# Kernel tuning notes

Measured on AMD Instinct MI355X. Metric: run time of the kernel, lower is better.

The kernel has to match this reference:

```python
import jax, jax.numpy as jnp
import numpy as np

N_COARSE = 100_000
M_FINE = 4 * N_COARSE
GRID = 128
C_IN, C_HID, C_OUT = 32, 64, 32
K3 = 27   # 3x3x3 neighborhood
K2 = 8    # 2x2x2 transposed-conv offsets


def setup_inputs() -> dict:
    rng = np.random.default_rng(0)
    # --- sparse coarse grid: N unique voxels in GRID^3 ---
    lin = np.sort(rng.choice(GRID ** 3, size=N_COARSE, replace=False))
    cx, cy, cz = lin // (GRID * GRID), (lin // GRID) % GRID, lin % GRID
    coords = np.stack([cx, cy, cz], 1).astype(np.int64)
    # --- rulebook: neighbor index per voxel per 3^3 offset (sentinel = N) ---
    offs = np.array([(dx, dy, dz) for dx in (-1, 0, 1) for dy in (-1, 0, 1) for dz in (-1, 0, 1)])
    nbr = np.full((N_COARSE, K3), N_COARSE, np.int32)
    for k in range(K3):
        nc = coords + offs[k]
        valid = ((nc >= 0) & (nc < GRID)).all(1)
        nlin = nc[:, 0] * GRID * GRID + nc[:, 1] * GRID + nc[:, 2]
        pos = np.clip(np.searchsorted(lin, nlin), 0, N_COARSE - 1)
        found = valid & (lin[pos] == nlin)
        nbr[found, k] = pos[found].astype(np.int32)
    # --- fine grid: 4 distinct children (of 8) per coarse voxel ---
    child = np.argsort(rng.random((N_COARSE, K2)), axis=1)[:, :4].astype(np.int32)
    parent_idx = np.repeat(np.arange(N_COARSE, dtype=np.int32), 4)
    offset_idx = child.reshape(-1)

    key = jax.random.key(0)
    ks = jax.random.split(key, 16)
    nrm = lambda k, sh, fan: (jax.random.normal(k, sh, jnp.float32) / np.sqrt(fan)).astype(jnp.float32)
    return {
        "feats_in": jax.random.normal(ks[0], (N_COARSE, C_IN), jnp.float32),
        "x_up_feats": jax.random.normal(ks[1], (M_FINE, C_OUT), jnp.float32),
        "nbr_idx": jnp.asarray(nbr),
        "parent_idx": jnp.asarray(parent_idx),
        "offset_idx": jnp.asarray(offset_idx),
        "W_enc1": nrm(ks[2], (K3, C_IN, C_HID), K3 * C_IN),
        "b_enc1": jnp.zeros((C_HID,), jnp.float32),
        "W_enc2": nrm(ks[3], (K3, C_HID, C_HID), K3 * C_HID),
        "b_enc2": jnp.zeros((C_HID,), jnp.float32),
        "W_enc3": nrm(ks[4], (K3, C_HID, C_HID), K3 * C_HID),
        "b_enc3": jnp.zeros((C_HID,), jnp.float32),
        "W_t": nrm(ks[5], (K2, C_HID, C_HID), C_HID),
        "b_t": jnp.zeros((C_HID,), jnp.float32),
        "W_d1": nrm(ks[6], (C_HID, C_HID), C_HID),
        "b_d1": jnp.zeros((C_HID,), jnp.float32),
        "W_d2": nrm(ks[7], (C_HID, C_OUT), C_HID),
        "b_d2": jnp.zeros((C_OUT,), jnp.float32),
    }


def _sparse_conv3(x, nbr, W, b):
    """3x3x3 stride-1 sparse conv: gather neighbors, per-offset matmul, accumulate.
    x: [N,Cin], nbr: [N,27] (sentinel N -> zero feature), W: [27,Cin,Cout]."""
    xp = jnp.concatenate([x, jnp.zeros((1, x.shape[1]), x.dtype)], 0)  # sentinel row
    acc = jnp.broadcast_to(b, (x.shape[0], W.shape[-1]))
    for k in range(W.shape[0]):  # fixed 27-way structural loop
        acc = acc + xp[nbr[:, k]] @ W[k]
    return acc


def _t_conv2(x, parent_idx, offset_idx, W, b):
    """2x2x2 stride-2 transposed sparse conv onto a given fine grid.
    x: [N,C], parent_idx: [M] (sentinel N), offset_idx: [M] in [0,8)."""
    xp = jnp.concatenate([x, jnp.zeros((1, x.shape[1]), x.dtype)], 0)
    g = xp[parent_idx]  # [M,C]
    out = jnp.broadcast_to(b, (g.shape[0], W.shape[-1]))
    for k in range(W.shape[0]):  # fixed 8-way structural loop
        out = out + jnp.where((offset_idx == k)[:, None], g @ W[k], 0.0)
    return out


def reference(feats_in, x_up_feats, nbr_idx, parent_idx, offset_idx,
              W_enc1, b_enc1, W_enc2, b_enc2, W_enc3, b_enc3,
              W_t, b_t, W_d1, b_d1, W_d2, b_d2):
    # encoder: (conv -> dropout[eval: identity] -> relu) x 3
    x = jax.nn.relu(_sparse_conv3(feats_in, nbr_idx, W_enc1, b_enc1))
    x = jax.nn.relu(_sparse_conv3(x, nbr_idx, W_enc2, b_enc2))
    x = jax.nn.relu(_sparse_conv3(x, nbr_idx, W_enc3, b_enc3))
    # transposed upsample conv onto x_upsample's grid
    x = _t_conv2(x, parent_idx, offset_idx, W_t, b_t)
    # decoder: relu -> 1x1 conv -> relu -> 1x1 conv, then residual add
    x = jax.nn.relu(x) @ W_d1 + b_d1
    x = jax.nn.relu(x) @ W_d2 + b_d2
    return x + x_up_feats
```

## Files before the change

kernel.cpp:

```cpp
#include <hip/hip_runtime.h>
#include <hip/hip_bf16.h>

#define NC 100000
#define MF 400000
#define K3 27

typedef __bf16 bf16_t;
typedef bf16_t bf16x8 __attribute__((ext_vector_type(8)));
typedef float  f32x4  __attribute__((ext_vector_type(4)));

#define O_E1 0
#define O_E2 55296
#define O_E3 165888
#define O_T  276480
#define O_D1 309248
#define O_D2 313344
#define W_TOTAL 315392

__device__ __align__(16) bf16_t g_w[W_TOTAL];
__device__ __align__(16) bf16_t g_x0[(size_t)NC * 32];
__device__ __align__(16) bf16_t g_x1[(size_t)NC * 64];
__device__ __align__(16) bf16_t g_x2[(size_t)NC * 64];
__device__ int g_nbrT[(size_t)K3 * NC];

static __device__ __forceinline__ bf16x8 zero8() {
    bf16x8 v;
#pragma unroll
    for (int i = 0; i < 8; ++i) v[i] = (bf16_t)0.0f;
    return v;
}

__global__ __launch_bounds__(256) void prep_k(
    const float* __restrict__ W_e1, const float* __restrict__ W_e2,
    const float* __restrict__ W_e3, const float* __restrict__ W_t,
    const float* __restrict__ W_d1, const float* __restrict__ W_d2,
    const float* __restrict__ feats, const int* __restrict__ nbr)
{
    int b = blockIdx.x;
    if (b < 154) {
        int tid = b * 256 + threadIdx.x;
        int lane = tid & 63;
        int f = tid >> 6;
        const float* src; int doff, nt, nc, fb;
        if      (f < 108) { src = W_e1; doff = O_E1; nt = 4; nc = 1; fb = 0;   }
        else if (f < 324) { src = W_e2; doff = O_E2; nt = 4; nc = 2; fb = 108; }
        else if (f < 540) { src = W_e3; doff = O_E3; nt = 4; nc = 2; fb = 324; }
        else if (f < 604) { src = W_t;  doff = O_T;  nt = 4; nc = 2; fb = 540; }
        else if (f < 612) { src = W_d1; doff = O_D1; nt = 4; nc = 2; fb = 604; }
        else              { src = W_d2; doff = O_D2; nt = 2; nc = 2; fb = 612; }
        int lf = f - fb;
        int t  = lf % nt;
        int c  = (lf / nt) % nc;
        int ko = lf / (nt * nc);
        int Cin = nc * 32, Cout = nt * 16;
        int n  = t * 16 + (lane & 15);
        int kb = c * 32 + (lane >> 4) * 8;
        bf16x8 tmp;
#pragma unroll
        for (int j = 0; j < 8; ++j)
            tmp[j] = (bf16_t)src[((size_t)ko * Cin + (kb + j)) * Cout + n];
        *(bf16x8*)(g_w + doff + (size_t)lf * 512 + lane * 8) = tmp;
    } else if (b < 1717) {
        int i = (b - 154) * 256 + threadIdx.x;
        if (i < NC * 32 / 8) {
            const f32x4* p = (const f32x4*)(feats + (size_t)i * 8);
            f32x4 lo = p[0], hi = p[1];
            bf16x8 v;
#pragma unroll
            for (int j = 0; j < 4; ++j) { v[j] = (bf16_t)lo[j]; v[j + 4] = (bf16_t)hi[j]; }
            *(bf16x8*)(g_x0 + (size_t)i * 8) = v;
        }
    } else {
        int r = (b - 1717) * 256 + threadIdx.x;
        if (r < NC) {
#pragma unroll
            for (int k = 0; k < K3; ++k)
                g_nbrT[(size_t)k * NC + r] = nbr[(size_t)r * K3 + k];
        }
    }
}

#define TS 72
template <int CH>
__global__ __launch_bounds__(128) void conv_k(
    int w_off,
    const float* __restrict__ bias,
    int src_sel, int dst_sel)
{
    constexpr int CIN = CH * 32;
    const bf16_t* xb = (src_sel == 0) ? g_x0 : (src_sel == 1 ? g_x1 : g_x2);
    bf16_t* y = (dst_sel == 1) ? g_x1 : g_x2;
    const bf16_t* wsrc = g_w + w_off;

    __shared__ __align__(16) bf16_t bB[2][4096];
    int tid = threadIdx.x;
    int wv = tid >> 6, lane = tid & 63;
    int cl = lane & 15, q = lane >> 4;

    int per = gridDim.x >> 3;
    int blk = (blockIdx.x & 7) * per + (blockIdx.x >> 3);
    int base = (blk * 2 + wv) * 64;

    {
        const bf16x8* s = (const bf16x8*)wsrc;
        bf16x8* d = (bf16x8*)bB[0];
#pragma unroll
        for (int i = 0; i < CH * 2; ++i) d[i * 128 + tid] = s[i * 128 + tid];
    }
    __syncthreads();

    f32x4 acc[4][4];
#pragma unroll
    for (int t = 0; t < 4; ++t) {
        float b = bias[t * 16 + cl];
#pragma unroll
        for (int mt = 0; mt < 4; ++mt) acc[mt][t] = (f32x4){b, b, b, b};
    }

    for (int ko = 0; ko < K3; ++ko) {
        int cur = ko & 1;
        if (ko + 1 < K3) {
            const bf16x8* s = (const bf16x8*)(wsrc + (size_t)(ko + 1) * CH * 2048);
            bf16x8* d = (bf16x8*)bB[cur ^ 1];
#pragma unroll
            for (int i = 0; i < CH * 2; ++i) d[i * 128 + tid] = s[i * 128 + tid];
        }
        int idx[4];
#pragma unroll
        for (int mt = 0; mt < 4; ++mt) {
            int r = base + mt * 16 + cl;
            idx[mt] = (r < NC) ? g_nbrT[(size_t)ko * NC + r] : NC;
        }
#pragma unroll
        for (int c = 0; c < CH; ++c) {
            bf16x8 bfr[4];
#pragma unroll
            for (int t = 0; t < 4; ++t)
                bfr[t] = *(const bf16x8*)&bB[cur][(c * 4 + t) * 512 + lane * 8];
#pragma unroll
            for (int mt = 0; mt < 4; ++mt) {
                bool valid = (unsigned)idx[mt] < (unsigned)NC;
                int s = valid ? idx[mt] : 0;
                bf16x8 a = *(const bf16x8*)(xb + (size_t)s * CIN + c * 32 + q * 8);
                if (!valid) a = zero8();
#pragma unroll
                for (int t = 0; t < 4; ++t)
                    acc[mt][t] = __builtin_amdgcn_mfma_f32_16x16x32_bf16(
                        a, bfr[t], acc[mt][t], 0, 0, 0);
            }
        }
        __syncthreads();
    }

    bf16_t* tb = ((bf16_t*)bB) + wv * 2304;
#pragma unroll
    for (int ch = 0; ch < 2; ++ch) {
#pragma unroll
        for (int mt2 = 0; mt2 < 2; ++mt2)
#pragma unroll
            for (int t = 0; t < 4; ++t)
#pragma unroll
                for (int r = 0; r < 4; ++r) {
                    float v = acc[ch * 2 + mt2][t][r];
                    v = v > 0.0f ? v : 0.0f;
                    tb[(mt2 * 16 + q * 4 + r) * TS + t * 16 + cl] = (bf16_t)v;
                }
#pragma unroll
        for (int i = 0; i < 4; ++i) {
            int rl = i * 8 + (lane >> 3);
            int c8 = (lane & 7) * 8;
            bf16x8 v8 = *(const bf16x8*)&tb[rl * TS + c8];
            int orow = base + ch * 32 + rl;
            if (orow < NC)
                *(bf16x8*)(y + (size_t)orow * 64 + c8) = v8;
        }
    }
}

#define HS 72
__global__ __launch_bounds__(256) void tconv_dec_k(
    const int*   __restrict__ offs,
    const float* __restrict__ b_t,
    const float* __restrict__ b_d1,
    const float* __restrict__ b_d2,
    const float* __restrict__ x_up,
    float*       __restrict__ out)
{
    __shared__ __align__(16) bf16_t h_lds[4][64 * HS];
    __shared__ __align__(16) int off_lds[4][64];
    int wv = threadIdx.x >> 6, lane = threadIdx.x & 63;
    int cl = lane & 15, q = lane >> 4;
    int per = gridDim.x >> 3;
    int blk = (blockIdx.x & 7) * per + (blockIdx.x >> 3);
    int p0 = (blk * 4 + wv) * 16;
    int fbase = p0 * 4;

    {
        int fi = fbase + lane;
        off_lds[wv][lane] = (fi < MF) ? offs[fi] : 0;
    }
    int code[4];
#pragma unroll
    for (int r = 0; r < 4; ++r) {
        int4 o = *(const int4*)&off_lds[wv][(q * 4 + r) * 4];
        code[r] = (1 << (4 * o.x)) | (2 << (4 * o.y)) |
                  (3 << (4 * o.z)) | (4 << (4 * o.w));
    }

    bool pv = (p0 + cl) < NC;
    size_t xrow = (size_t)(pv ? p0 + cl : 0) * 64;
    bf16x8 ax[2];
#pragma unroll
    for (int c = 0; c < 2; ++c) {
        bf16x8 t8 = *(const bf16x8*)(g_x1 + xrow + c * 32 + q * 8);
        ax[c] = pv ? t8 : zero8();
    }

    const bf16_t* wt = g_w + O_T;
#pragma unroll
    for (int k = 0; k < 8; ++k) {
        f32x4 acc[4];
#pragma unroll
        for (int t = 0; t < 4; ++t) {
            float b = b_t[t * 16 + cl];
            acc[t] = (f32x4){b, b, b, b};
        }
#pragma unroll
        for (int c = 0; c < 2; ++c) {
            const bf16_t* wb = wt + ((size_t)(k * 2 + c) * 4) * 512 + lane * 8;
#pragma unroll
            for (int t = 0; t < 4; ++t) {
                bf16x8 b = *(const bf16x8*)(wb + t * 512);
                acc[t] = __builtin_amdgcn_mfma_f32_16x16x32_bf16(ax[c], b, acc[t], 0, 0, 0);
            }
        }
#pragma unroll
        for (int r = 0; r < 4; ++r) {
            int nib = (code[r] >> (4 * k)) & 0xF;
            if (nib) {
                int fl = (((q * 4 + r) * 4) + (nib - 1)) & 63;
#pragma unroll
                for (int t = 0; t < 4; ++t) {
                    float v = acc[t][r];
                    v = v > 0.0f ? v : 0.0f;
                    h_lds[wv][fl * HS + t * 16 + cl] = (bf16_t)v;
                }
            }
        }
    }

    bf16x8 a1[4][2];
#pragma unroll
    for (int mt = 0; mt < 4; ++mt)
#pragma unroll
        for (int c = 0; c < 2; ++c)
            a1[mt][c] = *(const bf16x8*)&h_lds[wv][(mt * 16 + cl) * HS + c * 32 + q * 8];

#pragma unroll
    for (int mt = 0; mt < 4; ++mt) {
        f32x4 acc2[4];
#pragma unroll
        for (int t = 0; t < 4; ++t) {
            float b = b_d1[t * 16 + cl];
            acc2[t] = (f32x4){b, b, b, b};
        }
#pragma unroll
        for (int c = 0; c < 2; ++c)
#pragma unroll
            for (int t = 0; t < 4; ++t) {
                bf16x8 b = *(const bf16x8*)(g_w + O_D1 + (size_t)(c * 4 + t) * 512 + lane * 8);
                acc2[t] = __builtin_amdgcn_mfma_f32_16x16x32_bf16(a1[mt][c], b, acc2[t], 0, 0, 0);
            }
#pragma unroll
        for (int t = 0; t < 4; ++t)
#pragma unroll
            for (int r = 0; r < 4; ++r) {
                float v = acc2[t][r];
                v = v > 0.0f ? v : 0.0f;
                h_lds[wv][(mt * 16 + q * 4 + r) * HS + t * 16 + cl] = (bf16_t)v;
            }
    }

    float* fW = (float*)h_lds[wv];
#pragma unroll
    for (int mt = 0; mt < 4; ++mt) {
        bf16x8 a2[2];
#pragma unroll
        for (int c = 0; c < 2; ++c)
            a2[c] = *(const bf16x8*)&h_lds[wv][(mt * 16 + cl) * HS + c * 32 + q * 8];
        f32x4 acc3[2];
#pragma unroll
        for (int t = 0; t < 2; ++t) {
            float b = b_d2[t * 16 + cl];
            acc3[t] = (f32x4){b, b, b, b};
        }
#pragma unroll
        for (int c = 0; c < 2; ++c)
#pragma unroll
            for (int t = 0; t < 2; ++t) {
                bf16x8 b = *(const bf16x8*)(g_w + O_D2 + (size_t)(c * 2 + t) * 512 + lane * 8);
                acc3[t] = __builtin_amdgcn_mfma_f32_16x16x32_bf16(a2[c], b, acc3[t], 0, 0, 0);
            }
#pragma unroll
        for (int t = 0; t < 2; ++t)
#pragma unroll
            for (int r = 0; r < 4; ++r)
                fW[(mt * 16 + q * 4 + r) * 36 + t * 16 + cl] = acc3[t][r];
    }

#pragma unroll
    for (int i = 0; i < 8; ++i) {
        int rl = i * 8 + (lane >> 3);
        int c4 = (lane & 7) * 4;
        int fg = fbase + rl;
        if (fg < MF) {
            f32x4 xv = *(const f32x4*)(x_up + (size_t)fg * 32 + c4);
            f32x4 v = *(const f32x4*)&fW[rl * 36 + c4];
            v += xv;
            *(f32x4*)(out + (size_t)fg * 32 + c4) = v;
        }
    }
}

extern "C" void kernel_launch(void* const* d_in, const int* in_sizes, int n_in,
                              void* d_out, int out_size, void* d_ws, size_t ws_size,
                              hipStream_t stream) {
    const float* feats  = (const float*)d_in[0];
    const float* x_up   = (const float*)d_in[1];
    const int*   nbr    = (const int*)d_in[2];
    const int*   offs   = (const int*)d_in[4];
    const float* W_e1 = (const float*)d_in[5];
    const float* b_e1 = (const float*)d_in[6];
    const float* W_e2 = (const float*)d_in[7];
    const float* b_e2 = (const float*)d_in[8];
    const float* W_e3 = (const float*)d_in[9];
    const float* b_e3 = (const float*)d_in[10];
    const float* W_t  = (const float*)d_in[11];
    const float* b_t  = (const float*)d_in[12];
    const float* W_d1 = (const float*)d_in[13];
    const float* b_d1 = (const float*)d_in[14];
    const float* W_d2 = (const float*)d_in[15];
    const float* b_d2 = (const float*)d_in[16];
    float* out = (float*)d_out;

    prep_k<<<2108, 256, 0, stream>>>(W_e1, W_e2, W_e3, W_t, W_d1, W_d2, feats, nbr);

    conv_k<1><<<784, 128, 0, stream>>>(O_E1, b_e1, 0, 1);
    conv_k<2><<<784, 128, 0, stream>>>(O_E2, b_e2, 1, 2);
    conv_k<2><<<784, 128, 0, stream>>>(O_E3, b_e3, 2, 1);

    tconv_dec_k<<<1568, 256, 0, stream>>>(offs, b_t, b_d1, b_d2, x_up, out);
}
```

Measured before the change: 339.3 us.

## Software-pipeline neighbor gathers in sparse conv and prefetch residual input

The conv kernel now double-buffers the neighbor indices and the gathered activation fragments in registers, loading offset k+1's A tiles and offset k+2's indices while the MFMAs for offset k run. This is meant to hide the latency of the irregular global gathers. The launch bound adds a minimum-blocks hint of 1, and the extra register buffers may lower occupancy. The tconv/decoder kernel also loads the x_up residual at kernel start so that read overlaps with the compute.

Result: no change. 337.8 us (-0.4%).

```diff
diff --git a/kernel.cpp b/kernel.cpp
--- a/kernel.cpp
+++ b/kernel.cpp
@@ -81,8 +81,55 @@
 }
 
 #define TS 72
+
+#define CSTEP(KO, P) do {                                                      \
+    if ((KO) + 1 < K3) {                                                       \
+                            \
+        const bf16x8* s_ = (const bf16x8*)(wsrc + (size_t)((KO) + 1) * CH * 2048); \
+        bf16x8* d_ = (bf16x8*)bB[(P) ^ 1];                                     \
+        _Pragma("unroll")                                                      \
+        for (int i_ = 0; i_ < CH * 2; ++i_)                                    \
+            d_[i_ * 128 + tid] = s_[i_ * 128 + tid];                           \
+                 \
+        _Pragma("unroll")                                                      \
+        for (int c_ = 0; c_ < CH; ++c_)                                        \
+            _Pragma("unroll")                                                  \
+            for (int mt_ = 0; mt_ < 4; ++mt_) {                                \
+                int ii_ = idxbuf[(P) ^ 1][mt_];                                \
+                bool va_ = (unsigned)ii_ < (unsigned)NC;                       \
+                int ss_ = va_ ? ii_ : 0;                                       \
+                bf16x8 a_ = *(const bf16x8*)(xb + (size_t)ss_ * CIN + c_ * 32 + q * 8); \
+                if (!va_) a_ = zero8();                                        \
+                abuf[(P) ^ 1][c_][mt_] = a_;                                   \
+            }                                                                  \
+    }                                                                          \
+    if ((KO) + 2 < K3) {                                                       \
+                 \
+        _Pragma("unroll")                                                      \
+        for (int mt_ = 0; mt_ < 4; ++mt_) {                                    \
+            int r_ = base + mt_ * 16 + cl;                                     \
+            idxbuf[P][mt_] = (r_ < NC) ? g_nbrT[(size_t)((KO) + 2) * NC + r_] : NC; \
+        }                                                                      \
+    }                                                                          \
+                                        \
+    _Pragma("unroll")                                                          \
+    for (int c_ = 0; c_ < CH; ++c_) {                                          \
+        bf16x8 bfr_[4];                                                        \
+        _Pragma("unroll")                                                      \
+        for (int t_ = 0; t_ < 4; ++t_)                                         \
+            bfr_[t_] = *(const bf16x8*)&bB[P][(c_ * 4 + t_) * 512 + lane * 8]; \
+        _Pragma("unroll")                                                      \
+        for (int mt_ = 0; mt_ < 4; ++mt_)                                      \
+            _Pragma("unroll")                                                  \
+            for (int t_ = 0; t_ < 4; ++t_)                                     \
+                acc[mt_][t_] = __builtin_amdgcn_mfma_f32_16x16x32_bf16(        \
+                    abuf[P][c_][mt_], bfr_[t_], acc[mt_][t_], 0, 0, 0);        \
+    }                                                                          \
+    __syncthreads();                                                           \
+} while (0)
+
 template <int CH>
-__global__ __launch_bounds__(128) void conv_k(
+__global__ __launch_bounds__(128, 1) void conv_k(
     int w_off,
     const float* __restrict__ bias,
     int src_sel, int dst_sel)
@@ -107,7 +154,30 @@
 #pragma unroll
         for (int i = 0; i < CH * 2; ++i) d[i * 128 + tid] = s[i * 128 + tid];
     }
-    __syncthreads();
+
+    int idxbuf[2][4];
+    bf16x8 abuf[2][CH][4];
+#pragma unroll
+    for (int mt = 0; mt < 4; ++mt) {
+        int r = base + mt * 16 + cl;
+        idxbuf[0][mt] = (r < NC) ? g_nbrT[(size_t)0 * NC + r] : NC;
+    }
+#pragma unroll
+    for (int c = 0; c < CH; ++c)
+#pragma unroll
+        for (int mt = 0; mt < 4; ++mt) {
+            int ii = idxbuf[0][mt];
+            bool va = (unsigned)ii < (unsigned)NC;
+            int ss = va ? ii : 0;
+            bf16x8 a = *(const bf16x8*)(xb + (size_t)ss * CIN + c * 32 + q * 8);
+            if (!va) a = zero8();
+            abuf[0][c][mt] = a;
+        }
+#pragma unroll
+    for (int mt = 0; mt < 4; ++mt) {
+        int r = base + mt * 16 + cl;
+        idxbuf[1][mt] = (r < NC) ? g_nbrT[(size_t)1 * NC + r] : NC;
+    }
 
     f32x4 acc[4][4];
 #pragma unroll
@@ -116,41 +186,13 @@
 #pragma unroll
         for (int mt = 0; mt < 4; ++mt) acc[mt][t] = (f32x4){b, b, b, b};
     }
-
-    for (int ko = 0; ko < K3; ++ko) {
-        int cur = ko & 1;
-        if (ko + 1 < K3) {
-            const bf16x8* s = (const bf16x8*)(wsrc + (size_t)(ko + 1) * CH * 2048);
-            bf16x8* d = (bf16x8*)bB[cur ^ 1];
-#pragma unroll
-            for (int i = 0; i < CH * 2; ++i) d[i * 128 + tid] = s[i * 128 + tid];
-        }
-        int idx[4];
-#pragma unroll
-        for (int mt = 0; mt < 4; ++mt) {
-            int r = base + mt * 16 + cl;
-            idx[mt] = (r < NC) ? g_nbrT[(size_t)ko * NC + r] : NC;
-        }
-#pragma unroll
-        for (int c = 0; c < CH; ++c) {
-            bf16x8 bfr[4];
-#pragma unroll
-            for (int t = 0; t < 4; ++t)
-                bfr[t] = *(const bf16x8*)&bB[cur][(c * 4 + t) * 512 + lane * 8];
-#pragma unroll
-            for (int mt = 0; mt < 4; ++mt) {
-                bool valid = (unsigned)idx[mt] < (unsigned)NC;
-                int s = valid ? idx[mt] : 0;
-                bf16x8 a = *(const bf16x8*)(xb + (size_t)s * CIN + c * 32 + q * 8);
-                if (!valid) a = zero8();
-#pragma unroll
-                for (int t = 0; t < 4; ++t)
-                    acc[mt][t] = __builtin_amdgcn_mfma_f32_16x16x32_bf16(
-                        a, bfr[t], acc[mt][t], 0, 0, 0);
-            }
-        }
-        __syncthreads();
-    }
+    __syncthreads();
+
+    for (int ko = 0; ko < K3 - 1; ko += 2) {
+        CSTEP(ko, 0);
+        CSTEP(ko + 1, 1);
+    }
+    CSTEP(K3 - 1, 0);
 
     bf16_t* tb = ((bf16_t*)bB) + wv * 2304;
 #pragma unroll
@@ -195,6 +237,16 @@
     int p0 = (blk * 4 + wv) * 16;
     int fbase = p0 * 4;
 
+    f32x4 xup[8];
+#pragma unroll
+    for (int i = 0; i < 8; ++i) {
+        int rl = i * 8 + (lane >> 3);
+        int c4 = (lane & 7) * 4;
+        int fg = fbase + rl;
+        if (fg < MF) xup[i] = *(const f32x4*)(x_up + (size_t)fg * 32 + c4);
+        else         xup[i] = (f32x4){0.f, 0.f, 0.f, 0.f};
+    }
+
     {
         int fi = fbase + lane;
         off_lds[wv][lane] = (fi < MF) ? offs[fi] : 0;
@@ -314,9 +366,8 @@
         int c4 = (lane & 7) * 4;
         int fg = fbase + rl;
         if (fg < MF) {
-            f32x4 xv = *(const f32x4*)(x_up + (size_t)fg * 32 + c4);
             f32x4 v = *(const f32x4*)&fW[rl * 36 + c4];
-            v += xv;
+            v += xup[i];
             *(f32x4*)(out + (size_t)fg * 32 + c4) = v;
         }
     }
```
